# Kernel tuning notes

Hardware: AMD Instinct MI355X
Metric: run time of the kernel (lower is better)

The kernel has to match this reference:

```python
import jax, jax.numpy as jnp
import numpy as np

F, H, D, A, B = 500, 2000, 64, 64, 4096


def setup_inputs() -> dict:
    key = jax.random.key(0)
    ks = jax.random.split(key, 6)
    values = jax.random.normal(ks[0], (B, F), dtype=jnp.float32)
    feat_emb = jax.random.normal(ks[1], (F, D), dtype=jnp.float32) * 0.02
    hid_emb = jax.random.normal(ks[2], (H, D), dtype=jnp.float32) * 0.02
    Ww = jax.random.normal(ks[3], (2 * D, A), dtype=jnp.float32) * (1.0 / np.sqrt(2 * D))
    bw = jnp.zeros((A,), dtype=jnp.float32)
    Wu = jax.random.normal(ks[4], (A, 1), dtype=jnp.float32) * (1.0 / np.sqrt(A))
    mask = jax.random.bernoulli(ks[5], 0.1, (F, F + H, 1))
    return {"values": values, "feat_emb": feat_emb, "hid_emb": hid_emb,
            "Ww": Ww, "bw": bw, "Wu": Wu, "mask": mask}


def reference(values, feat_emb, hid_emb, Ww, bw, Wu, mask):
    d = feat_emb.shape[1]
    # full embedding matrix: concat(feature, hidden) -> [F+H, d]
    full = jnp.concatenate([feat_emb, hid_emb], axis=0)
    # Dense(tanh) on concat([feat_emb tiled, full tiled], axis=2) == split-weight form:
    # avoids materializing the [F, F+H, 2d] concat tensor (same math).
    W1, W2 = Ww[:d], Ww[d:]
    pre_f = feat_emb @ W1          # [F, A]
    pre_w = full @ W2              # [F+H, A]
    h = jnp.tanh(pre_f[:, None, :] + pre_w[None, :, :] + bw)  # [F, F+H, A]
    score = h @ Wu                 # [F, F+H, 1]
    # masked exp-normalize (not a stable softmax: original uses raw exp)
    score = jnp.where(mask, jnp.exp(score), 0.0)
    ssum = jnp.sum(score, axis=1, keepdims=True)        # [F, 1, 1]
    ssum = jnp.where(ssum == 0, 1.0, ssum)
    attn = score / ssum                                  # [F, F+H, 1]
    context = jnp.sum(attn * full[None, :, :], axis=1)   # [F, d]
    return values @ context                              # [B, d]
```

## Files before the change

kernel.cpp:

```cpp
#include <hip/hip_runtime.h>
#include <cstdint>
#include <cstddef>

#define F_N 500
#define H_N 2000
#define JN  2500
#define D_N 64
#define A_N 64
#define B_N 4096

#define SPLIT  4
#define JCHUNK 625

__global__ __launch_bounds__(256) void k_pre(
    const float* __restrict__ feat, const float* __restrict__ hid,
    const float* __restrict__ Ww,   const float* __restrict__ bw,
    float* __restrict__ pre_f, float* __restrict__ pre_w,
    float* __restrict__ zero_region)
{
    const int gt = blockIdx.x * 256 + threadIdx.x;
    if (gt < 32512) zero_region[gt] = 0.0f;

    const int lane = threadIdx.x & 63;
    const int wave = threadIdx.x >> 6;
    int row = blockIdx.x * 4 + wave;
    row = __builtin_amdgcn_readfirstlane(row);
    if (row >= F_N + JN) return;

    const float* emb;
    const float* W;
    float*       outp;
    float acc0, acc1 = 0.0f;

    if (row < F_N) {
        emb  = feat + (size_t)row * D_N;
        W    = Ww;
        outp = pre_f + (size_t)row * A_N;
        acc0 = bw[lane];
    } else {
        const int j = row - F_N;
        emb  = (j < F_N) ? (feat + (size_t)j * D_N)
                         : (hid + (size_t)(j - F_N) * D_N);
        W    = Ww + D_N * A_N;
        outp = pre_w + (size_t)j * A_N;
        acc0 = 0.0f;
    }

    #pragma unroll
    for (int d = 0; d < D_N; d += 2) {
        acc0 = fmaf(emb[d],     W[(d    ) * A_N + lane], acc0);
        acc1 = fmaf(emb[d + 1], W[(d + 1) * A_N + lane], acc1);
    }
    outp[lane] = acc0 + acc1;
}

__global__ __launch_bounds__(256, 8) void k_attn(
    const float* __restrict__ feat, const float* __restrict__ hid,
    const float* __restrict__ pre_f, const float* __restrict__ pre_w,
    const float* __restrict__ Wu,   const void* __restrict__ mask,
    float* __restrict__ csum, float* __restrict__ esum)
{
    const int tid  = threadIdx.x;
    const int lane = tid & 63;
    const int wave = tid >> 6;
    const int i    = blockIdx.x >> 2;
    const int sub  = blockIdx.x & 3;
    const int jbase = sub * JCHUNK;

    __shared__ int   list[JCHUNK];
    __shared__ float earr[JCHUNK];
    __shared__ float s_ctx[4][64];
    __shared__ int   nact;

    if (tid == 0) nact = 0;
    __syncthreads();

    const uint32_t* mw = (const uint32_t*)mask;
    const uint32_t probe = mw[lane] | mw[64 + lane] | mw[128 + lane] | mw[192 + lane];
    const bool byteMode = (__ballot(probe > 1u) != 0ull);

    const uint8_t*  mb = (const uint8_t*)mask + (size_t)i * JN + jbase;
    const uint32_t* mi = (const uint32_t*)mask + (size_t)i * JN + jbase;

    for (int t = tid; t < 768; t += 256) {
        uint32_t m = 0;
        if (t < JCHUNK) m = byteMode ? (uint32_t)mb[t] : mi[t];
        const unsigned long long act = __ballot(m != 0);
        const int cnt = __popcll(act);
        int base = 0;
        if (lane == 0 && cnt) base = atomicAdd(&nact, cnt);
        base = __shfl(base, 0, 64);
        if (m) {
            const int rank = __popcll(act & ((1ull << lane) - 1ull));
            list[base + rank] = jbase + t;
        }
    }
    __syncthreads();
    const int n = nact;

    const float* pf = pre_f + (size_t)i * A_N;
    for (int idx = tid; idx < n; idx += 256) {
        const int j = list[idx];
        const float4* pwj = (const float4*)(pre_w + (size_t)j * A_N);
        float s0 = 0.0f, s1 = 0.0f, s2 = 0.0f, s3 = 0.0f;
        #pragma unroll
        for (int q = 0; q < 16; ++q) {
            const float4 v = pwj[q];
            const int a = q * 4;
            const float x0 = pf[a + 0] + v.x;
            const float x1 = pf[a + 1] + v.y;
            const float x2 = pf[a + 2] + v.z;
            const float x3 = pf[a + 3] + v.w;
            const float t0 = fmaf(-2.0f, __builtin_amdgcn_rcpf(__expf(2.0f * x0) + 1.0f), 1.0f);
            const float t1 = fmaf(-2.0f, __builtin_amdgcn_rcpf(__expf(2.0f * x1) + 1.0f), 1.0f);
            const float t2 = fmaf(-2.0f, __builtin_amdgcn_rcpf(__expf(2.0f * x2) + 1.0f), 1.0f);
            const float t3 = fmaf(-2.0f, __builtin_amdgcn_rcpf(__expf(2.0f * x3) + 1.0f), 1.0f);
            s0 = fmaf(Wu[a + 0], t0, s0);
            s1 = fmaf(Wu[a + 1], t1, s1);
            s2 = fmaf(Wu[a + 2], t2, s2);
            s3 = fmaf(Wu[a + 3], t3, s3);
        }
        earr[idx] = __expf((s0 + s1) + (s2 + s3));
    }
    __syncthreads();

    float cacc = 0.0f;
    int idx = wave;
    for (; idx + 12 < n; idx += 16) {
        const float e0 = earr[idx];      const int j0 = list[idx];
        const float e1 = earr[idx + 4];  const int j1 = list[idx + 4];
        const float e2 = earr[idx + 8];  const int j2 = list[idx + 8];
        const float e3 = earr[idx + 12]; const int j3 = list[idx + 12];
        const float* r0 = (j0 < F_N) ? (feat + (size_t)j0 * D_N) : (hid + (size_t)(j0 - F_N) * D_N);
        const float* r1 = (j1 < F_N) ? (feat + (size_t)j1 * D_N) : (hid + (size_t)(j1 - F_N) * D_N);
        const float* r2 = (j2 < F_N) ? (feat + (size_t)j2 * D_N) : (hid + (size_t)(j2 - F_N) * D_N);
        const float* r3 = (j3 < F_N) ? (feat + (size_t)j3 * D_N) : (hid + (size_t)(j3 - F_N) * D_N);
        const float v0 = r0[lane];
        const float v1 = r1[lane];
        const float v2 = r2[lane];
        const float v3 = r3[lane];
        cacc = fmaf(e0, v0, cacc);
        cacc = fmaf(e1, v1, cacc);
        cacc = fmaf(e2, v2, cacc);
        cacc = fmaf(e3, v3, cacc);
    }
    for (; idx < n; idx += 4) {
        const float e = earr[idx];
        const int   j = list[idx];
        const float* row = (j < F_N) ? (feat + (size_t)j * D_N)
                                     : (hid + (size_t)(j - F_N) * D_N);
        cacc = fmaf(e, row[lane], cacc);
    }
    s_ctx[wave][lane] = cacc;
    __syncthreads();

    if (wave == 0) {
        const float c4 = s_ctx[0][lane] + s_ctx[1][lane] + s_ctx[2][lane] + s_ctx[3][lane];
        float ss = 0.0f;
        for (int k = lane; k < n; k += 64) ss += earr[k];
        #pragma unroll
        for (int off = 1; off < 64; off <<= 1) ss += __shfl_xor(ss, off, 64);
        atomicAdd(&csum[(size_t)i * D_N + lane], c4);
        if (lane == 0) atomicAdd(&esum[i], ss);
    }
}

__global__ __launch_bounds__(256) void k_out(
    const float* __restrict__ values, const float* __restrict__ csum,
    const float* __restrict__ esum,   float* __restrict__ out)
{
    const int tid  = threadIdx.x;
    const int lane = tid & 63;
    const int wave = tid >> 6;
    int r0 = blockIdx.x * 8 + wave * 2;
    r0 = __builtin_amdgcn_readfirstlane(r0);

    __shared__ float ctx_l[100 * 64];

    float4 cbuf[7];
    float  ebuf[7];

    float acc0 = 0.0f, acc1 = 0.0f;

    {
        const float4* cp = (const float4*)csum;
        #pragma unroll
        for (int q = 0; q < 7; ++q) {
            const int t = tid + q * 256;
            if (t < 1600) { cbuf[q] = cp[t]; ebuf[q] = esum[t >> 4]; }
        }
    }

    for (int chunk = 0; chunk < 5; ++chunk) {
        __syncthreads();
        {
            float4* cl = (float4*)ctx_l;
            #pragma unroll
            for (int q = 0; q < 7; ++q) {
                const int t = tid + q * 256;
                if (t < 1600) {
                    const float e   = ebuf[q];
                    const float inv = (e == 0.0f) ? 1.0f : __builtin_amdgcn_rcpf(e);
                    float4 c = cbuf[q];
                    c.x *= inv; c.y *= inv; c.z *= inv; c.w *= inv;
                    cl[t] = c;
                }
            }
        }
        __syncthreads();

        if (chunk < 4) {
            const int k0n = (chunk + 1) * 100;
            const float4* cp = (const float4*)(csum + (size_t)k0n * 64);
            #pragma unroll
            for (int q = 0; q < 7; ++q) {
                const int t = tid + q * 256;
                if (t < 1600) { cbuf[q] = cp[t]; ebuf[q] = esum[k0n + (t >> 4)]; }
            }
        }

        const int k0 = chunk * 100;
        const float* v0 = values + (size_t)(r0 + 0) * 500 + k0;
        const float* v1 = values + (size_t)(r0 + 1) * 500 + k0;
        #pragma unroll 10
        for (int k = 0; k < 100; k += 4) {
            const float c0 = ctx_l[(k + 0) * 64 + lane];
            const float c1 = ctx_l[(k + 1) * 64 + lane];
            const float c2 = ctx_l[(k + 2) * 64 + lane];
            const float c3 = ctx_l[(k + 3) * 64 + lane];
            acc0 = fmaf(v0[k + 0], c0, acc0); acc0 = fmaf(v0[k + 1], c1, acc0);
            acc0 = fmaf(v0[k + 2], c2, acc0); acc0 = fmaf(v0[k + 3], c3, acc0);
            acc1 = fmaf(v1[k + 0], c0, acc1); acc1 = fmaf(v1[k + 1], c1, acc1);
            acc1 = fmaf(v1[k + 2], c2, acc1); acc1 = fmaf(v1[k + 3], c3, acc1);
        }
    }

    out[(size_t)(r0 + 0) * 64 + lane] = acc0;
    out[(size_t)(r0 + 1) * 64 + lane] = acc1;
}

extern "C" void kernel_launch(void* const* d_in, const int* in_sizes, int n_in,
                              void* d_out, int out_size, void* d_ws, size_t ws_size,
                              hipStream_t stream)
{
    const float* values = (const float*)d_in[0];
    const float* feat   = (const float*)d_in[1];
    const float* hid    = (const float*)d_in[2];
    const float* Ww     = (const float*)d_in[3];
    const float* bw     = (const float*)d_in[4];
    const float* Wu     = (const float*)d_in[5];
    const void*  mask   = d_in[6];
    float* out = (float*)d_out;

    float* wsf   = (float*)d_ws;
    float* pre_f = wsf;
    float* pre_w = wsf + 32000;
    float* csum  = wsf + 192000;
    float* esum  = wsf + 224000;

    k_pre <<<750,  256, 0, stream>>>(feat, hid, Ww, bw, pre_f, pre_w, csum);
    k_attn<<<2000, 256, 0, stream>>>(feat, hid, pre_f, pre_w, Wu, mask, csum, esum);
    k_out <<<512,  256, 0, stream>>>(values, csum, esum, out);
}
```

Baseline: 110.4 us.

## Halve attention j-split and replace atomics with per-split partial buffers

Each attention block now covers half of the F+H range instead of a quarter, so the grid shrinks from 2000 to 1000 blocks. Each block writes its context and exp-sum partials to its own slot rather than using atomicAdd into a shared accumulator. That removes the zeroing pass in k_pre and the atomic contention. The output kernel then loads both partials and sums them before normalizing. The cost is fewer, longer attention blocks (lower parallelism, larger shared-memory lists) and twice the csum loads in k_out.

```diff
diff --git a/kernel.cpp b/kernel.cpp
--- a/kernel.cpp
+++ b/kernel.cpp
@@ -9,18 +9,14 @@
 #define A_N 64
 #define B_N 4096
 
-#define SPLIT  4
-#define JCHUNK 625
+#define SPLIT  2
+#define JCHUNK 1250
 
 __global__ __launch_bounds__(256) void k_pre(
     const float* __restrict__ feat, const float* __restrict__ hid,
     const float* __restrict__ Ww,   const float* __restrict__ bw,
-    float* __restrict__ pre_f, float* __restrict__ pre_w,
-    float* __restrict__ zero_region)
-{
-    const int gt = blockIdx.x * 256 + threadIdx.x;
-    if (gt < 32512) zero_region[gt] = 0.0f;
-
+    float* __restrict__ pre_f, float* __restrict__ pre_w)
+{
     const int lane = threadIdx.x & 63;
     const int wave = threadIdx.x >> 6;
     int row = blockIdx.x * 4 + wave;
@@ -63,8 +59,8 @@
     const int tid  = threadIdx.x;
     const int lane = tid & 63;
     const int wave = tid >> 6;
-    const int i    = blockIdx.x >> 2;
-    const int sub  = blockIdx.x & 3;
+    const int i    = blockIdx.x >> 1;
+    const int sub  = blockIdx.x & 1;
     const int jbase = sub * JCHUNK;
 
     __shared__ int   list[JCHUNK];
@@ -82,7 +78,7 @@
     const uint8_t*  mb = (const uint8_t*)mask + (size_t)i * JN + jbase;
     const uint32_t* mi = (const uint32_t*)mask + (size_t)i * JN + jbase;
 
-    for (int t = tid; t < 768; t += 256) {
+    for (int t = tid; t < 1280; t += 256) {
         uint32_t m = 0;
         if (t < JCHUNK) m = byteMode ? (uint32_t)mb[t] : mi[t];
         const unsigned long long act = __ballot(m != 0);
@@ -160,8 +156,8 @@
         for (int k = lane; k < n; k += 64) ss += earr[k];
         #pragma unroll
         for (int off = 1; off < 64; off <<= 1) ss += __shfl_xor(ss, off, 64);
-        atomicAdd(&csum[(size_t)i * D_N + lane], c4);
-        if (lane == 0) atomicAdd(&esum[i], ss);
+        csum[((size_t)sub * F_N + i) * D_N + lane] = c4;
+        if (lane == 0) esum[sub * F_N + i] = ss;
     }
 }
 
@@ -177,17 +173,22 @@
 
     __shared__ float ctx_l[100 * 64];
 
-    float4 cbuf[7];
+    float4 cbuf0[7], cbuf1[7];
     float  ebuf[7];
 
     float acc0 = 0.0f, acc1 = 0.0f;
 
     {
-        const float4* cp = (const float4*)csum;
+        const float4* cp0 = (const float4*)csum;
+        const float4* cp1 = (const float4*)(csum + (size_t)F_N * D_N);
         #pragma unroll
         for (int q = 0; q < 7; ++q) {
             const int t = tid + q * 256;
-            if (t < 1600) { cbuf[q] = cp[t]; ebuf[q] = esum[t >> 4]; }
+            if (t < 1600) {
+                cbuf0[q] = cp0[t];
+                cbuf1[q] = cp1[t];
+                ebuf[q]  = esum[t >> 4] + esum[F_N + (t >> 4)];
+            }
         }
     }
 
@@ -201,8 +202,11 @@
                 if (t < 1600) {
                     const float e   = ebuf[q];
                     const float inv = (e == 0.0f) ? 1.0f : __builtin_amdgcn_rcpf(e);
-                    float4 c = cbuf[q];
-                    c.x *= inv; c.y *= inv; c.z *= inv; c.w *= inv;
+                    float4 c;
+                    c.x = (cbuf0[q].x + cbuf1[q].x) * inv;
+                    c.y = (cbuf0[q].y + cbuf1[q].y) * inv;
+                    c.z = (cbuf0[q].z + cbuf1[q].z) * inv;
+                    c.w = (cbuf0[q].w + cbuf1[q].w) * inv;
                     cl[t] = c;
                 }
             }
@@ -211,11 +215,16 @@
 
         if (chunk < 4) {
             const int k0n = (chunk + 1) * 100;
-            const float4* cp = (const float4*)(csum + (size_t)k0n * 64);
+            const float4* cp0 = (const float4*)(csum + (size_t)k0n * 64);
+            const float4* cp1 = (const float4*)(csum + (size_t)(F_N + k0n) * 64);
             #pragma unroll
             for (int q = 0; q < 7; ++q) {
                 const int t = tid + q * 256;
-                if (t < 1600) { cbuf[q] = cp[t]; ebuf[q] = esum[k0n + (t >> 4)]; }
+                if (t < 1600) {
+                    cbuf0[q] = cp0[t];
+                    cbuf1[q] = cp1[t];
+                    ebuf[q]  = esum[k0n + (t >> 4)] + esum[F_N + k0n + (t >> 4)];
+                }
             }
         }
 
@@ -256,9 +265,9 @@
     float* pre_f = wsf;
     float* pre_w = wsf + 32000;
     float* csum  = wsf + 192000;
-    float* esum  = wsf + 224000;
-
-    k_pre <<<750,  256, 0, stream>>>(feat, hid, Ww, bw, pre_f, pre_w, csum);
-    k_attn<<<2000, 256, 0, stream>>>(feat, hid, pre_f, pre_w, Wu, mask, csum, esum);
+    float* esum  = wsf + 256000;
+
+    k_pre <<<750,  256, 0, stream>>>(feat, hid, Ww, bw, pre_f, pre_w);
+    k_attn<<<1000, 256, 0, stream>>>(feat, hid, pre_f, pre_w, Wu, mask, csum, esum);
     k_out <<<512,  256, 0, stream>>>(values, csum, esum, out);
 }
```

Result: slower. 113.6 us (+2.9%).
